# Kernel tuning notes

Hardware: AMD Instinct MI355X
Metric: run time of the kernel (lower is better)

The kernel has to match this reference:

```python
import jax, jax.numpy as jnp
import numpy as np

MARGIN = 1.0
CONTR_LAMDA = 100.0
GN_LAMDA = 0.3
IMG_SCALE = 2
EPS = 1e-9


def bilinear(fmap, pts):
    # fmap: (B,C,H,W); pts: (B,N,2) as (x,y). Returns (B*N, C).
    B, C, H, W = fmap.shape
    N = pts.shape[1]
    x = jnp.clip(pts[..., 0], 0.0, W - 1.0)
    y = jnp.clip(pts[..., 1], 0.0, H - 1.0)
    x0 = jnp.floor(x)
    y0 = jnp.floor(y)
    wx = (x - x0)[:, None, :]
    wy = (y - y0)[:, None, :]
    x0i = x0.astype(jnp.int32)
    y0i = y0.astype(jnp.int32)
    x1i = jnp.minimum(x0i + 1, W - 1)
    y1i = jnp.minimum(y0i + 1, H - 1)
    fm = fmap.reshape(B, C, H * W)

    def gather(yi, xi):
        idx = yi * W + xi  # (B,N)
        idx = jnp.broadcast_to(idx[:, None, :], (B, C, N))
        return jnp.take_along_axis(fm, idx, axis=2)  # (B,C,N)

    v = (gather(y0i, x0i) * (1 - wx) * (1 - wy)
         + gather(y0i, x1i) * wx * (1 - wy)
         + gather(y1i, x0i) * (1 - wx) * wy
         + gather(y1i, x1i) * wx * wy)
    return v.transpose(0, 2, 1).reshape(B * N, C)


def grad2d(f):
    # central differences with edge replication (torch_gradient)
    fx = jnp.pad(f, ((0, 0), (0, 0), (0, 0), (1, 1)), mode='edge')
    gx = 0.5 * (fx[..., 2:] - fx[..., :-2])
    fy = jnp.pad(f, ((0, 0), (0, 0), (1, 1), (0, 0)), mode='edge')
    gy = 0.5 * (fy[..., 2:, :] - fy[..., :-2, :])
    return gx, gy


def gn_loss(f_t, fb, ub, noise):
    # f_t: (B*N,C); fb: (B,C,H,W); ub,noise: (B,N,2)
    B, N, _ = ub.shape
    xs = noise + ub
    f_s = bilinear(fb, xs)
    r = f_s - f_t  # (BN, C) residual
    gx, gy = grad2d(fb)
    Jx = bilinear(gx, xs)  # (BN, C)
    Jy = bilinear(gy, xs)
    # H = J^T J + eps*I  -- closed-form batched 2x2
    a = jnp.sum(Jx * Jx, axis=1) + EPS
    d = jnp.sum(Jy * Jy, axis=1) + EPS
    b = jnp.sum(Jx * Jy, axis=1)
    det = a * d - b * b
    bx = jnp.sum(Jx * r, axis=1)
    by = jnp.sum(Jy * r, axis=1)
    # Hinv @ (J^T r)
    ix = (d * bx - b * by) / det
    iy = (-b * bx + a * by) / det
    miu = xs.reshape(B * N, 2) - jnp.stack([ix, iy], axis=-1)
    du = ub.reshape(B * N, 2) - miu
    q = a * du[:, 0] ** 2 + 2.0 * b * du[:, 0] * du[:, 1] + d * du[:, 1] ** 2
    e1 = 0.5 * jnp.sum(q)
    e2 = B * N * jnp.log(jnp.asarray(2.0 * np.pi, jnp.float32)) - 0.5 * jnp.sum(jnp.log(det))
    return e1 + 2.0 * e2 / 7.0


def triplet_loss(fa_map, fb_map, ma, mb, ng):
    fa = bilinear(fa_map, ma)
    fp = bilinear(fb_map, mb)
    fn = bilinear(fb_map, ng)
    dp = jnp.linalg.norm(fa - fp, axis=1)
    dn = jnp.linalg.norm(fa - fn, axis=1)
    return jnp.mean(jax.nn.relu(dp - dn + MARGIN))


def setup_inputs() -> dict:
    key = jax.random.key(0)
    ks = jax.random.split(key, 16)
    B, C, N = 4, 32, 2048
    sizes = [64, 128, 256, 512]
    d = {}
    for i, h in enumerate(sizes):
        d[f'fa{i}'] = jax.random.normal(ks[i], (B, C, h, h), jnp.float32)
        d[f'fb{i}'] = jax.random.normal(ks[4 + i], (B, C, h, h), jnp.float32)
        d[f'noise{i}'] = jax.random.normal(ks[8 + i], (B, N, 2), jnp.float32)
    d['ma'] = jax.random.uniform(ks[12], (B, N, 2), jnp.float32) * 1024.0
    d['mb'] = jax.random.uniform(ks[13], (B, N, 2), jnp.float32) * 1024.0
    d['neg'] = jax.random.uniform(ks[14], (B, N, 2), jnp.float32) * 1024.0
    d['epoch'] = 5
    return d


def reference(fa0, fa1, fa2, fa3, fb0, fb1, fb2, fb3,
              noise0, noise1, noise2, noise3, ma, mb, neg, epoch):
    Fa = [fa0, fa1, fa2, fa3]
    Fb = [fb0, fb1, fb2, fb3]
    noises = [noise0, noise1, noise2, noise3]
    loss = jnp.float32(0.0)
    tl = jnp.float32(0.0)
    gl = jnp.float32(0.0)
    for i in range(4):
        level = 2 ** (3 - i)
        s = float(level * IMG_SCALE)
        f_t = bilinear(Fa[i], ma / s)
        lt = triplet_loss(Fa[i], Fb[i], ma / s, mb / s, neg / s)
        lg = gn_loss(f_t, Fb[i], mb / s, noises[i])
        loss = loss + CONTR_LAMDA * lt + GN_LAMDA * lg
        tl = tl + CONTR_LAMDA * lt
        gl = gl + GN_LAMDA * lg
    return loss, tl, gl
```

## Files before the change

### kernel.cpp

```cpp
#include <hip/hip_runtime.h>
#include <math.h>


struct BL { int x0, x1, y0, y1; float wx, wy; };
struct LevelPtrs { const float* fa[4]; const float* fb[4]; const float* nz[4]; };

__device__ __forceinline__ float2 load2u(const float* p) { float2 v; __builtin_memcpy(&v, p, 8); return v; }
__device__ __forceinline__ float4 load4u(const float* p) { float4 v; __builtin_memcpy(&v, p, 16); return v; }

__device__ __forceinline__ BL bl_setup(float px, float py, int W, int H) {
    BL r;
    float x = fminf(fmaxf(px, 0.0f), (float)(W - 1));
    float y = fminf(fmaxf(py, 0.0f), (float)(H - 1));
    float fx = floorf(x), fy = floorf(y);
    r.wx = x - fx; r.wy = y - fy;
    r.x0 = (int)fx; r.y0 = (int)fy;
    r.x1 = min(r.x0 + 1, W - 1);
    r.y1 = min(r.y0 + 1, H - 1);
    return r;
}

__device__ __forceinline__ float bl_eval_slow(const float* __restrict__ f, int W, const BL& s) {
    float v00 = f[s.y0 * W + s.x0];
    float v01 = f[s.y0 * W + s.x1];
    float v10 = f[s.y1 * W + s.x0];
    float v11 = f[s.y1 * W + s.x1];
    float a0 = v00 + s.wx * (v01 - v00);
    float a1 = v10 + s.wx * (v11 - v10);
    return a0 + s.wy * (a1 - a0);
}

__device__ __forceinline__ void j_eval_slow(const float* __restrict__ f, int W, int H,
                                            const BL& s, float& Jx, float& Jy) {
    int xR0 = min(s.x0 + 1, W - 1), xL0 = max(s.x0 - 1, 0);
    int xR1 = min(s.x1 + 1, W - 1), xL1 = max(s.x1 - 1, 0);
    int yD0 = min(s.y0 + 1, H - 1), yU0 = max(s.y0 - 1, 0);
    int yD1 = min(s.y1 + 1, H - 1), yU1 = max(s.y1 - 1, 0);
    const float* r0 = f + s.y0 * W;
    const float* r1 = f + s.y1 * W;
    float gx00 = r0[xR0] - r0[xL0];
    float gx01 = r0[xR1] - r0[xL1];
    float gx10 = r1[xR0] - r1[xL0];
    float gx11 = r1[xR1] - r1[xL1];
    float gy00 = f[yD0 * W + s.x0] - f[yU0 * W + s.x0];
    float gy01 = f[yD0 * W + s.x1] - f[yU0 * W + s.x1];
    float gy10 = f[yD1 * W + s.x0] - f[yU1 * W + s.x0];
    float gy11 = f[yD1 * W + s.x1] - f[yU1 * W + s.x1];
    float g0 = gx00 + s.wx * (gx01 - gx00);
    float g1 = gx10 + s.wx * (gx11 - gx10);
    Jx = 0.5f * (g0 + s.wy * (g1 - g0));
    float h0 = gy00 + s.wx * (gy01 - gy00);
    float h1 = gy10 + s.wx * (gy11 - gy10);
    Jy = 0.5f * (h0 + s.wy * (h1 - h0));
}

__device__ __forceinline__ float warp32_sum(float v) {
    v += __shfl_xor(v, 16);
    v += __shfl_xor(v, 8);
    v += __shfl_xor(v, 4);
    v += __shfl_xor(v, 2);
    v += __shfl_xor(v, 1);
    return v;
}

__global__ __launch_bounds__(1024) void sort_points_kernel(
    const float* __restrict__ mb, int* __restrict__ perm) {
    const int b = blockIdx.x;
    __shared__ unsigned int keys[2048];
    const float* mbb = mb + (size_t)b * 2048 * 2;
    for (int i = threadIdx.x; i < 2048; i += 1024) {
        int ix = min(max((int)mbb[i * 2 + 0], 0), 1023);
        int iy = min(max((int)mbb[i * 2 + 1], 0), 1023);
        unsigned m = 0;
        #pragma unroll
        for (int t = 0; t < 10; ++t)
            m |= (((unsigned)(ix >> t) & 1u) << (2 * t)) | (((unsigned)(iy >> t) & 1u) << (2 * t + 1));
        keys[i] = (m << 11) | (unsigned)i;
    }
    __syncthreads();
    for (unsigned k = 2; k <= 2048; k <<= 1) {
        for (unsigned j = k >> 1; j > 0; j >>= 1) {
            unsigned t = threadIdx.x;
            unsigned i1 = 2 * t - (t & (j - 1));
            unsigned i2 = i1 + j;
            bool up = ((i1 & k) == 0);
            unsigned a = keys[i1], c = keys[i2];
            if ((a > c) == up) { keys[i1] = c; keys[i2] = a; }
            __syncthreads();
        }
    }
    for (int i = threadIdx.x; i < 2048; i += 1024)
        perm[b * 2048 + i] = (int)(keys[i] & 2047u);
}

struct Task {
    const float* fac;
    const float* fbc;
    BL sa, sb, sg, sx;
    float nzx, nzy;
    bool fast;
    float2 va0, va1, vb0, vb1, vg0, vg1;
    float4 xm, x0, x1, x2;
    float fav, fpv, fnv, fsv, Jx, Jy;
};

__device__ __forceinline__ void task_setup(Task& T, int rank, const int* __restrict__ perm,
                                           const LevelPtrs& P, int lvl, int c, int W, int H,
                                           float inv_s,
                                           const float* __restrict__ ma,
                                           const float* __restrict__ mb,
                                           const float* __restrict__ ng) {
    const int b = rank >> 11;
    const int n = perm ? perm[rank] : (rank & 2047);
    const int q = (b << 11) + n;
    const int HW = H * W;
    T.fac = P.fa[lvl] + (size_t)(b * 32 + c) * HW;
    T.fbc = P.fb[lvl] + (size_t)(b * 32 + c) * HW;
    const float* noise = P.nz[lvl];
    const int p2 = q * 2;
    T.nzx = noise[p2]; T.nzy = noise[p2 + 1];
    const float pax = ma[p2] * inv_s, pay = ma[p2 + 1] * inv_s;
    const float pbx = mb[p2] * inv_s, pby = mb[p2 + 1] * inv_s;
    const float pnx = ng[p2] * inv_s, pny = ng[p2 + 1] * inv_s;
    const float xsx = T.nzx + pbx, xsy = T.nzy + pby;
    T.sa = bl_setup(pax, pay, W, H);
    T.sb = bl_setup(pbx, pby, W, H);
    T.sg = bl_setup(pnx, pny, W, H);
    T.sx = bl_setup(xsx, xsy, W, H);
    T.fast = (T.sa.x0 < W - 1) & (T.sb.x0 < W - 1) & (T.sg.x0 < W - 1) &
             (T.sx.x0 >= 1) & (T.sx.x0 <= W - 3) & (T.sx.y0 >= 1) & (T.sx.y0 <= H - 3);
}

__device__ __forceinline__ void task_issue(Task& T, int W, int H) {
    if (T.fast) {
        const float* xbp = T.fbc + (T.sx.y0 - 1) * W + (T.sx.x0 - 1);
        T.va0 = load2u(T.fac + T.sa.y0 * W + T.sa.x0);
        T.va1 = load2u(T.fac + T.sa.y1 * W + T.sa.x0);
        T.vb0 = load2u(T.fbc + T.sb.y0 * W + T.sb.x0);
        T.vb1 = load2u(T.fbc + T.sb.y1 * W + T.sb.x0);
        T.vg0 = load2u(T.fbc + T.sg.y0 * W + T.sg.x0);
        T.vg1 = load2u(T.fbc + T.sg.y1 * W + T.sg.x0);
        T.xm = load4u(xbp);
        T.x0 = load4u(xbp + W);
        T.x1 = load4u(xbp + 2 * W);
        T.x2 = load4u(xbp + 3 * W);
    } else {
        T.fav = bl_eval_slow(T.fac, W, T.sa);
        T.fpv = bl_eval_slow(T.fbc, W, T.sb);
        T.fnv = bl_eval_slow(T.fbc, W, T.sg);
        T.fsv = bl_eval_slow(T.fbc, W, T.sx);
        j_eval_slow(T.fbc, W, H, T.sx, T.Jx, T.Jy);
    }
}

__device__ __forceinline__ void task_consume(Task& T) {
    if (T.fast) {
        {
            float t0 = T.va0.x + T.sa.wx * (T.va0.y - T.va0.x);
            float t1 = T.va1.x + T.sa.wx * (T.va1.y - T.va1.x);
            T.fav = t0 + T.sa.wy * (t1 - t0);
        }
        {
            float t0 = T.vb0.x + T.sb.wx * (T.vb0.y - T.vb0.x);
            float t1 = T.vb1.x + T.sb.wx * (T.vb1.y - T.vb1.x);
            T.fpv = t0 + T.sb.wy * (t1 - t0);
        }
        {
            float t0 = T.vg0.x + T.sg.wx * (T.vg0.y - T.vg0.x);
            float t1 = T.vg1.x + T.sg.wx * (T.vg1.y - T.vg1.x);
            T.fnv = t0 + T.sg.wy * (t1 - t0);
        }
        {
            float wx = T.sx.wx, wy = T.sx.wy;
            float t0 = T.x0.y + wx * (T.x0.z - T.x0.y);
            float t1 = T.x1.y + wx * (T.x1.z - T.x1.y);
            T.fsv = t0 + wy * (t1 - t0);
            float gx00 = T.x0.z - T.x0.x, gx01 = T.x0.w - T.x0.y;
            float gx10 = T.x1.z - T.x1.x, gx11 = T.x1.w - T.x1.y;
            float gy00 = T.x1.y - T.xm.y, gy01 = T.x1.z - T.xm.z;
            float gy10 = T.x2.y - T.x0.y, gy11 = T.x2.z - T.x0.z;
            float g0 = gx00 + wx * (gx01 - gx00);
            float g1 = gx10 + wx * (gx11 - gx10);
            T.Jx = 0.5f * (g0 + wy * (g1 - g0));
            float h0 = gy00 + wx * (gy01 - gy00);
            float h1 = gy10 + wx * (gy11 - gy10);
            T.Jy = 0.5f * (h0 + wy * (h1 - h0));
        }
    }
}

__device__ __forceinline__ void task_reduce(const Task& T, int c, float* red0,
                                            float* red1, float* red2, int slot2) {
    float r = T.fsv - T.fav;
    float a  = warp32_sum(T.Jx * T.Jx);
    float dd = warp32_sum(T.Jy * T.Jy);
    float bb = warp32_sum(T.Jx * T.Jy);
    float bx = warp32_sum(T.Jx * r);
    float by = warp32_sum(T.Jy * r);
    float dfp = T.fav - T.fpv, dfn = T.fav - T.fnv;
    float sp = warp32_sum(dfp * dfp);
    float sn = warp32_sum(dfn * dfn);
    if (c == 0) {
        a += 1e-9f; dd += 1e-9f;
        float det = a * dd - bb * bb;
        float ix = (dd * bx - bb * by) / det;
        float iy = (a * by - bb * bx) / det;
        float dux = ix - T.nzx;
        float duy = iy - T.nzy;
        float qv = a * dux * dux + 2.0f * bb * dux * duy + dd * duy * duy;
        red0[slot2] = fmaxf(sqrtf(sp) - sqrtf(sn) + 1.0f, 0.0f);
        red1[slot2] = qv;
        red2[slot2] = logf(det);
    }
}

__global__ __launch_bounds__(256) void gn_fused_kernel(
    LevelPtrs P, const float* __restrict__ ma, const float* __restrict__ mb,
    const float* __restrict__ ng, const int* __restrict__ perm,
    float* __restrict__ blk_out) {
    const int tid = threadIdx.x;
    const int c = tid & 31;
    const int slot = tid >> 5;
    const int lvl = slot >> 1;
    const int po = slot & 1;
    const int bid = blockIdx.x;
    const int s_blk = ((bid & 7) << 8) + (bid >> 3);
    const int base = s_blk * 4;
    const int H = 64 << lvl;
    const int W = H;
    const float inv_s = 0.0625f * (float)(1 << lvl);

    Task T0, T1;
    task_setup(T0, base + po,     perm, P, lvl, c, W, H, inv_s, ma, mb, ng);
    task_setup(T1, base + 2 + po, perm, P, lvl, c, W, H, inv_s, ma, mb, ng);
    task_issue(T0, W, H);
    task_issue(T1, W, H);
    task_consume(T0);
    task_consume(T1);

    __shared__ float red[3][16];
    task_reduce(T0, c, red[0], red[1], red[2], slot * 2 + 0);
    task_reduce(T1, c, red[0], red[1], red[2], slot * 2 + 1);
    __syncthreads();
    if (tid == 0) {
        float t = 0.0f, qq = 0.0f, l = 0.0f;
        #pragma unroll
        for (int i = 0; i < 16; ++i) { t += red[0][i]; qq += red[1][i]; l += red[2][i]; }
        blk_out[bid * 3 + 0] = t;
        blk_out[bid * 3 + 1] = qq;
        blk_out[bid * 3 + 2] = l;
    }
}

__global__ __launch_bounds__(256) void gn_final_kernel(
    const float* __restrict__ part, int nblk, float* __restrict__ out) {
    __shared__ double sd[3][256];
    double st = 0.0, sq = 0.0, sl = 0.0;
    for (int i = threadIdx.x; i < nblk; i += 256) {
        st += (double)part[i * 3 + 0];
        sq += (double)part[i * 3 + 1];
        sl += (double)part[i * 3 + 2];
    }
    sd[0][threadIdx.x] = st; sd[1][threadIdx.x] = sq; sd[2][threadIdx.x] = sl;
    __syncthreads();
    for (int s = 128; s > 0; s >>= 1) {
        if (threadIdx.x < s) {
            sd[0][threadIdx.x] += sd[0][threadIdx.x + s];
            sd[1][threadIdx.x] += sd[1][threadIdx.x + s];
            sd[2][threadIdx.x] += sd[2][threadIdx.x + s];
        }
        __syncthreads();
    }
    if (threadIdx.x == 0) {
        double S_t = sd[0][0], S_q = sd[1][0], S_l = sd[2][0];
        double tl = 100.0 * S_t / 8192.0;
        double e2 = 4.0 * 8192.0 * 1.8378770664093453 - 0.5 * S_l;
        double gl = 0.3 * (0.5 * S_q + (2.0 / 7.0) * e2);
        out[0] = (float)(tl + gl);
        out[1] = (float)tl;
        out[2] = (float)gl;
    }
}

extern "C" void kernel_launch(void* const* d_in, const int* in_sizes, int n_in,
                              void* d_out, int out_size, void* d_ws, size_t ws_size,
                              hipStream_t stream) {
    const bool dict_order = (in_sizes[1] == in_sizes[0]);
    LevelPtrs P;
    for (int i = 0; i < 4; ++i) {
        if (dict_order) {
            P.fa[i] = (const float*)d_in[3 * i + 0];
            P.fb[i] = (const float*)d_in[3 * i + 1];
            P.nz[i] = (const float*)d_in[3 * i + 2];
        } else {
            P.fa[i] = (const float*)d_in[i];
            P.fb[i] = (const float*)d_in[4 + i];
            P.nz[i] = (const float*)d_in[8 + i];
        }
    }
    const float* ma = (const float*)d_in[12];
    const float* mb = (const float*)d_in[13];
    const float* ng = (const float*)d_in[14];

    float* ws = (float*)d_ws;
    const int nblk = 2048;
    float* partials = ws;
    int* perm = (int*)(ws + nblk * 3);
    const bool do_sort = ws_size >= (size_t)(nblk * 3 + 8192) * 4;

    if (do_sort) sort_points_kernel<<<4, 1024, 0, stream>>>(mb, perm);
    gn_fused_kernel<<<nblk, 256, 0, stream>>>(P, ma, mb, ng, do_sort ? perm : nullptr, partials);
    gn_final_kernel<<<1, 256, 0, stream>>>(partials, nblk, (float*)d_out);
}
```

Measured before the change: 110.3 us.

## Split gather into sorted per-coordinate passes with workspace staging of features

```diff
diff --git a/kernel.cpp b/kernel.cpp
--- a/kernel.cpp
+++ b/kernel.cpp
@@ -8,15 +8,17 @@
 __device__ __forceinline__ float2 load2u(const float* p) { float2 v; __builtin_memcpy(&v, p, 8); return v; }
 __device__ __forceinline__ float4 load4u(const float* p) { float4 v; __builtin_memcpy(&v, p, 16); return v; }
 
-__device__ __forceinline__ BL bl_setup(float px, float py, int W, int H) {
+__device__ __forceinline__ BL bl_setup2(float px, float py, int W, int H) {
     BL r;
     float x = fminf(fmaxf(px, 0.0f), (float)(W - 1));
     float y = fminf(fmaxf(py, 0.0f), (float)(H - 1));
     float fx = floorf(x), fy = floorf(y);
     r.wx = x - fx; r.wy = y - fy;
     r.x0 = (int)fx; r.y0 = (int)fy;
-    r.x1 = min(r.x0 + 1, W - 1);
-    r.y1 = min(r.y0 + 1, H - 1);
+    if (r.x0 >= W - 1) { r.x0 = W - 2; r.wx = 1.0f; }
+    if (r.y0 >= H - 1) { r.y0 = H - 2; r.wy = 1.0f; }
+    r.x1 = r.x0 + 1;
+    r.y1 = r.y0 + 1;
     return r;
 }
 
@@ -54,6 +56,16 @@
     Jy = 0.5f * (h0 + s.wy * (h1 - h0));
 }
 
+__device__ __forceinline__ float wave64_sum(float v) {
+    v += __shfl_xor(v, 32);
+    v += __shfl_xor(v, 16);
+    v += __shfl_xor(v, 8);
+    v += __shfl_xor(v, 4);
+    v += __shfl_xor(v, 2);
+    v += __shfl_xor(v, 1);
+    return v;
+}
+
 __device__ __forceinline__ float warp32_sum(float v) {
     v += __shfl_xor(v, 16);
     v += __shfl_xor(v, 8);
@@ -63,14 +75,17 @@
     return v;
 }
 
-__global__ __launch_bounds__(1024) void sort_points_kernel(
-    const float* __restrict__ mb, int* __restrict__ perm) {
-    const int b = blockIdx.x;
+__global__ __launch_bounds__(1024) void sort3_kernel(
+    const float* __restrict__ ma, const float* __restrict__ mb,
+    const float* __restrict__ ng, int* __restrict__ perm) {
+    const int cid = blockIdx.x >> 2;
+    const int b = blockIdx.x & 3;
+    const float* coords = (cid == 0) ? ma : (cid == 1) ? mb : ng;
     __shared__ unsigned int keys[2048];
-    const float* mbb = mb + (size_t)b * 2048 * 2;
+    const float* cb = coords + (size_t)b * 2048 * 2;
     for (int i = threadIdx.x; i < 2048; i += 1024) {
-        int ix = min(max((int)mbb[i * 2 + 0], 0), 1023);
-        int iy = min(max((int)mbb[i * 2 + 1], 0), 1023);
+        int ix = min(max((int)cb[i * 2 + 0], 0), 1023);
+        int iy = min(max((int)cb[i * 2 + 1], 0), 1023);
         unsigned m = 0;
         #pragma unroll
         for (int t = 0; t < 10; ++t)
@@ -90,7 +105,203 @@
         }
     }
     for (int i = threadIdx.x; i < 2048; i += 1024)
-        perm[b * 2048 + i] = (int)(keys[i] & 2047u);
+        perm[cid * 8192 + b * 2048 + i] = (int)(keys[i] & 2047u);
+}
+
+__global__ __launch_bounds__(256) void gather_pass_kernel(
+    LevelPtrs P, const float* __restrict__ ma, const float* __restrict__ ng,
+    const int* __restrict__ perm, float* __restrict__ ft, float* __restrict__ fn) {
+    const int bid = blockIdx.x;
+    const int role = bid & 1;
+    const int r = bid >> 1;
+    const int lvl = 3 - (r >> 7);
+    const int g = r & 127;
+    const int tid = threadIdx.x;
+    const int lane = tid & 63, w = tid >> 6, ch0 = w * 8;
+    const int rank = g * 64 + lane;
+    const int b = rank >> 11;
+    const int* pm = perm + (role ? 2 * 8192 : 0);
+    const int q = (b << 11) + pm[rank];
+    const int H = 64 << lvl, W = H, HW = H * W;
+    const float inv_s = 0.0625f * (float)(1 << lvl);
+    const float* coords = role ? ng : ma;
+    const float px = coords[q * 2] * inv_s, py = coords[q * 2 + 1] * inv_s;
+    BL s = bl_setup2(px, py, W, H);
+    const float* src = role ? P.fb[lvl] : P.fa[lvl];
+    const float* base = src + (size_t)(b * 32 + ch0) * HW + s.y0 * W + s.x0;
+
+    float2 v0[8], v1[8];
+    #pragma unroll
+    for (int cc = 0; cc < 8; ++cc) {
+        v0[cc] = load2u(base + (size_t)cc * HW);
+        v1[cc] = load2u(base + (size_t)cc * HW + W);
+    }
+    float out[8];
+    #pragma unroll
+    for (int cc = 0; cc < 8; ++cc) {
+        float t0 = v0[cc].x + s.wx * (v0[cc].y - v0[cc].x);
+        float t1 = v1[cc].x + s.wx * (v1[cc].y - v1[cc].x);
+        out[cc] = t0 + s.wy * (t1 - t0);
+    }
+    float* dst = (role ? fn : ft) + ((size_t)lvl * 8192 + q) * 32 + ch0;
+    float4 o0 = {out[0], out[1], out[2], out[3]};
+    float4 o1 = {out[4], out[5], out[6], out[7]};
+    *(float4*)dst = o0;
+    *(float4*)(dst + 4) = o1;
+}
+
+__device__ __forceinline__ void consume_ch(
+    const float* __restrict__ plane, int W, int H, const BL& sb, const BL& sx,
+    bool interior, float2 m0, float2 m1,
+    float4 r0, float4 r1, float4 r2, float4 r3,
+    float ftv, float fnv,
+    float& sp, float& sn, float& aa, float& dd, float& bb, float& bx, float& by) {
+    float t0 = m0.x + sb.wx * (m0.y - m0.x);
+    float t1 = m1.x + sb.wx * (m1.y - m1.x);
+    float fpv = t0 + sb.wy * (t1 - t0);
+    float fsv, Jx, Jy;
+    if (interior) {
+        float wx = sx.wx, wy = sx.wy;
+        float a0 = r1.y + wx * (r1.z - r1.y);
+        float a1 = r2.y + wx * (r2.z - r2.y);
+        fsv = a0 + wy * (a1 - a0);
+        float gx00 = r1.z - r1.x, gx01 = r1.w - r1.y;
+        float gx10 = r2.z - r2.x, gx11 = r2.w - r2.y;
+        float gy00 = r2.y - r0.y, gy01 = r2.z - r0.z;
+        float gy10 = r3.y - r1.y, gy11 = r3.z - r1.z;
+        float g0 = gx00 + wx * (gx01 - gx00);
+        float g1 = gx10 + wx * (gx11 - gx10);
+        Jx = 0.5f * (g0 + wy * (g1 - g0));
+        float h0 = gy00 + wx * (gy01 - gy00);
+        float h1 = gy10 + wx * (gy11 - gy10);
+        Jy = 0.5f * (h0 + wy * (h1 - h0));
+    } else {
+        fsv = bl_eval_slow(plane, W, sx);
+        j_eval_slow(plane, W, H, sx, Jx, Jy);
+    }
+    float rr = fsv - ftv;
+    float dp = ftv - fpv, dn = ftv - fnv;
+    sp += dp * dp;
+    sn += dn * dn;
+    aa += Jx * Jx;
+    dd += Jy * Jy;
+    bb += Jx * Jy;
+    bx += Jx * rr;
+    by += Jy * rr;
+}
+
+__global__ __launch_bounds__(256) void gn_main_kernel(
+    LevelPtrs P, const float* __restrict__ mb, const int* __restrict__ perm_mb,
+    const float* __restrict__ ft, const float* __restrict__ fn,
+    float* __restrict__ blk_out) {
+    const int bid = blockIdx.x;
+    const int lvl = 3 - (bid >> 7);
+    const int g = bid & 127;
+    const int tid = threadIdx.x;
+    const int lane = tid & 63, w = tid >> 6, ch0 = w * 8;
+    const int rank = g * 64 + lane;
+    const int b = rank >> 11;
+    const int q = (b << 11) + perm_mb[rank];
+    const int H = 64 << lvl, W = H, HW = H * W;
+    const float inv_s = 0.0625f * (float)(1 << lvl);
+    const float* noise = P.nz[lvl];
+    const int p2 = q * 2;
+    const float nzx = noise[p2], nzy = noise[p2 + 1];
+    const float pbx = mb[p2] * inv_s, pby = mb[p2 + 1] * inv_s;
+    const float xsx = nzx + pbx, xsy = nzy + pby;
+    BL sb = bl_setup2(pbx, pby, W, H);
+    BL sx = bl_setup2(xsx, xsy, W, H);
+    const bool interior = (sx.x0 >= 1) & (sx.x0 <= W - 3) & (sx.y0 >= 1) & (sx.y0 <= H - 3);
+    const int pbx0 = min(max(sx.x0 - 1, 0), W - 4);
+    const int pby0 = min(max(sx.y0 - 1, 0), H - 4);
+    const float* fb0 = P.fb[lvl] + (size_t)(b * 32 + ch0) * HW;
+
+    const float* ftp = ft + ((size_t)lvl * 8192 + q) * 32 + ch0;
+    const float* fnp = fn + ((size_t)lvl * 8192 + q) * 32 + ch0;
+    float4 ftA = *(const float4*)ftp, ftB = *(const float4*)(ftp + 4);
+    float4 fnA = *(const float4*)fnp, fnB = *(const float4*)(fnp + 4);
+    float ftv[8] = {ftA.x, ftA.y, ftA.z, ftA.w, ftB.x, ftB.y, ftB.z, ftB.w};
+    float fnv[8] = {fnA.x, fnA.y, fnA.z, fnA.w, fnB.x, fnB.y, fnB.z, fnB.w};
+
+    float sp = 0, sn = 0, aa = 0, dd = 0, bb = 0, bx = 0, by = 0;
+    const int mboff0 = sb.y0 * W + sb.x0;
+    const int pboff = pby0 * W + pbx0;
+    #pragma unroll
+    for (int cc = 0; cc < 8; cc += 2) {
+        const float* p0 = fb0 + (size_t)cc * HW;
+        const float* p1 = p0 + HW;
+        float2 m00 = load2u(p0 + mboff0);
+        float2 m01 = load2u(p0 + mboff0 + W);
+        float2 m10 = load2u(p1 + mboff0);
+        float2 m11 = load2u(p1 + mboff0 + W);
+        const float* xb0 = p0 + pboff;
+        const float* xb1 = p1 + pboff;
+        float4 r00 = load4u(xb0), r01 = load4u(xb0 + W), r02 = load4u(xb0 + 2 * W), r03 = load4u(xb0 + 3 * W);
+        float4 r10 = load4u(xb1), r11 = load4u(xb1 + W), r12 = load4u(xb1 + 2 * W), r13 = load4u(xb1 + 3 * W);
+        consume_ch(p0, W, H, sb, sx, interior, m00, m01, r00, r01, r02, r03,
+                   ftv[cc], fnv[cc], sp, sn, aa, dd, bb, bx, by);
+        consume_ch(p1, W, H, sb, sx, interior, m10, m11, r10, r11, r12, r13,
+                   ftv[cc + 1], fnv[cc + 1], sp, sn, aa, dd, bb, bx, by);
+    }
+
+    __shared__ float red[4][64][7];
+    red[w][lane][0] = sp; red[w][lane][1] = sn; red[w][lane][2] = aa;
+    red[w][lane][3] = dd; red[w][lane][4] = bb; red[w][lane][5] = bx;
+    red[w][lane][6] = by;
+    __syncthreads();
+    if (tid < 64) {
+        float t[7];
+        #pragma unroll
+        for (int k = 0; k < 7; ++k)
+            t[k] = red[0][tid][k] + red[1][tid][k] + red[2][tid][k] + red[3][tid][k];
+        float a2 = t[2] + 1e-9f, d2 = t[3] + 1e-9f, b2 = t[4];
+        float det = a2 * d2 - b2 * b2;
+        float ix = (d2 * t[5] - b2 * t[6]) / det;
+        float iy = (a2 * t[6] - b2 * t[5]) / det;
+        float dux = ix - nzx;
+        float duy = iy - nzy;
+        float qv = a2 * dux * dux + 2.0f * b2 * dux * duy + d2 * duy * duy;
+        float trip = fmaxf(sqrtf(t[0]) - sqrtf(t[1]) + 1.0f, 0.0f);
+        float ld = logf(det);
+        trip = wave64_sum(trip);
+        qv = wave64_sum(qv);
+        ld = wave64_sum(ld);
+        if (tid == 0) {
+            blk_out[bid * 3 + 0] = trip;
+            blk_out[bid * 3 + 1] = qv;
+            blk_out[bid * 3 + 2] = ld;
+        }
+    }
+}
+
+__global__ __launch_bounds__(256) void gn_final_kernel(
+    const float* __restrict__ part, int nblk, float* __restrict__ out) {
+    __shared__ double sd[3][256];
+    double st = 0.0, sq = 0.0, sl = 0.0;
+    for (int i = threadIdx.x; i < nblk; i += 256) {
+        st += (double)part[i * 3 + 0];
+        sq += (double)part[i * 3 + 1];
+        sl += (double)part[i * 3 + 2];
+    }
+    sd[0][threadIdx.x] = st; sd[1][threadIdx.x] = sq; sd[2][threadIdx.x] = sl;
+    __syncthreads();
+    for (int s = 128; s > 0; s >>= 1) {
+        if (threadIdx.x < s) {
+            sd[0][threadIdx.x] += sd[0][threadIdx.x + s];
+            sd[1][threadIdx.x] += sd[1][threadIdx.x + s];
+            sd[2][threadIdx.x] += sd[2][threadIdx.x + s];
+        }
+        __syncthreads();
+    }
+    if (threadIdx.x == 0) {
+        double S_t = sd[0][0], S_q = sd[1][0], S_l = sd[2][0];
+        double tl = 100.0 * S_t / 8192.0;
+        double e2 = 4.0 * 8192.0 * 1.8378770664093453 - 0.5 * S_l;
+        double gl = 0.3 * (0.5 * S_q + (2.0 / 7.0) * e2);
+        out[0] = (float)(tl + gl);
+        out[1] = (float)tl;
+        out[2] = (float)gl;
+    }
 }
 
 struct Task {
@@ -104,15 +315,13 @@
     float fav, fpv, fnv, fsv, Jx, Jy;
 };
 
-__device__ __forceinline__ void task_setup(Task& T, int rank, const int* __restrict__ perm,
-                                           const LevelPtrs& P, int lvl, int c, int W, int H,
-                                           float inv_s,
+__device__ __forceinline__ void task_setup(Task& T, int rank, const LevelPtrs& P,
+                                           int lvl, int c, int W, int H, float inv_s,
                                            const float* __restrict__ ma,
                                            const float* __restrict__ mb,
                                            const float* __restrict__ ng) {
     const int b = rank >> 11;
-    const int n = perm ? perm[rank] : (rank & 2047);
-    const int q = (b << 11) + n;
+    const int q = rank;
     const int HW = H * W;
     T.fac = P.fa[lvl] + (size_t)(b * 32 + c) * HW;
     T.fbc = P.fb[lvl] + (size_t)(b * 32 + c) * HW;
@@ -123,69 +332,63 @@
     const float pbx = mb[p2] * inv_s, pby = mb[p2 + 1] * inv_s;
     const float pnx = ng[p2] * inv_s, pny = ng[p2 + 1] * inv_s;
     const float xsx = T.nzx + pbx, xsy = T.nzy + pby;
-    T.sa = bl_setup(pax, pay, W, H);
-    T.sb = bl_setup(pbx, pby, W, H);
-    T.sg = bl_setup(pnx, pny, W, H);
-    T.sx = bl_setup(xsx, xsy, W, H);
-    T.fast = (T.sa.x0 < W - 1) & (T.sb.x0 < W - 1) & (T.sg.x0 < W - 1) &
-             (T.sx.x0 >= 1) & (T.sx.x0 <= W - 3) & (T.sx.y0 >= 1) & (T.sx.y0 <= H - 3);
+    T.sa = bl_setup2(pax, pay, W, H);
+    T.sb = bl_setup2(pbx, pby, W, H);
+    T.sg = bl_setup2(pnx, pny, W, H);
+    T.sx = bl_setup2(xsx, xsy, W, H);
+    T.fast = (T.sx.x0 >= 1) & (T.sx.x0 <= W - 3) & (T.sx.y0 >= 1) & (T.sx.y0 <= H - 3);
 }
 
 __device__ __forceinline__ void task_issue(Task& T, int W, int H) {
+    T.va0 = load2u(T.fac + T.sa.y0 * W + T.sa.x0);
+    T.va1 = load2u(T.fac + T.sa.y1 * W + T.sa.x0);
+    T.vb0 = load2u(T.fbc + T.sb.y0 * W + T.sb.x0);
+    T.vb1 = load2u(T.fbc + T.sb.y1 * W + T.sb.x0);
+    T.vg0 = load2u(T.fbc + T.sg.y0 * W + T.sg.x0);
+    T.vg1 = load2u(T.fbc + T.sg.y1 * W + T.sg.x0);
+    int bx0 = min(max(T.sx.x0 - 1, 0), W - 4);
+    int by0 = min(max(T.sx.y0 - 1, 0), H - 4);
+    const float* xbp = T.fbc + by0 * W + bx0;
+    T.xm = load4u(xbp);
+    T.x0 = load4u(xbp + W);
+    T.x1 = load4u(xbp + 2 * W);
+    T.x2 = load4u(xbp + 3 * W);
+}
+
+__device__ __forceinline__ void task_consume(Task& T, int W, int H) {
+    {
+        float t0 = T.va0.x + T.sa.wx * (T.va0.y - T.va0.x);
+        float t1 = T.va1.x + T.sa.wx * (T.va1.y - T.va1.x);
+        T.fav = t0 + T.sa.wy * (t1 - t0);
+    }
+    {
+        float t0 = T.vb0.x + T.sb.wx * (T.vb0.y - T.vb0.x);
+        float t1 = T.vb1.x + T.sb.wx * (T.vb1.y - T.vb1.x);
+        T.fpv = t0 + T.sb.wy * (t1 - t0);
+    }
+    {
+        float t0 = T.vg0.x + T.sg.wx * (T.vg0.y - T.vg0.x);
+        float t1 = T.vg1.x + T.sg.wx * (T.vg1.y - T.vg1.x);
+        T.fnv = t0 + T.sg.wy * (t1 - t0);
+    }
     if (T.fast) {
-        const float* xbp = T.fbc + (T.sx.y0 - 1) * W + (T.sx.x0 - 1);
-        T.va0 = load2u(T.fac + T.sa.y0 * W + T.sa.x0);
-        T.va1 = load2u(T.fac + T.sa.y1 * W + T.sa.x0);
-        T.vb0 = load2u(T.fbc + T.sb.y0 * W + T.sb.x0);
-        T.vb1 = load2u(T.fbc + T.sb.y1 * W + T.sb.x0);
-        T.vg0 = load2u(T.fbc + T.sg.y0 * W + T.sg.x0);
-        T.vg1 = load2u(T.fbc + T.sg.y1 * W + T.sg.x0);
-        T.xm = load4u(xbp);
-        T.x0 = load4u(xbp + W);
-        T.x1 = load4u(xbp + 2 * W);
-        T.x2 = load4u(xbp + 3 * W);
+        float wx = T.sx.wx, wy = T.sx.wy;
+        float t0 = T.x0.y + wx * (T.x0.z - T.x0.y);
+        float t1 = T.x1.y + wx * (T.x1.z - T.x1.y);
+        T.fsv = t0 + wy * (t1 - t0);
+        float gx00 = T.x0.z - T.x0.x, gx01 = T.x0.w - T.x0.y;
+        float gx10 = T.x1.z - T.x1.x, gx11 = T.x1.w - T.x1.y;
+        float gy00 = T.x1.y - T.xm.y, gy01 = T.x1.z - T.xm.z;
+        float gy10 = T.x2.y - T.x0.y, gy11 = T.x2.z - T.x0.z;
+        float g0 = gx00 + wx * (gx01 - gx00);
+        float g1 = gx10 + wx * (gx11 - gx10);
+        T.Jx = 0.5f * (g0 + wy * (g1 - g0));
+        float h0 = gy00 + wx * (gy01 - gy00);
+        float h1 = gy10 + wx * (gy11 - gy10);
+        T.Jy = 0.5f * (h0 + wy * (h1 - h0));
     } else {
-        T.fav = bl_eval_slow(T.fac, W, T.sa);
-        T.fpv = bl_eval_slow(T.fbc, W, T.sb);
-        T.fnv = bl_eval_slow(T.fbc, W, T.sg);
         T.fsv = bl_eval_slow(T.fbc, W, T.sx);
         j_eval_slow(T.fbc, W, H, T.sx, T.Jx, T.Jy);
-    }
-}
-
-__device__ __forceinline__ void task_consume(Task& T) {
-    if (T.fast) {
-        {
-            float t0 = T.va0.x + T.sa.wx * (T.va0.y - T.va0.x);
-            float t1 = T.va1.x + T.sa.wx * (T.va1.y - T.va1.x);
-            T.fav = t0 + T.sa.wy * (t1 - t0);
-        }
-        {
-            float t0 = T.vb0.x + T.sb.wx * (T.vb0.y - T.vb0.x);
-            float t1 = T.vb1.x + T.sb.wx * (T.vb1.y - T.vb1.x);
-            T.fpv = t0 + T.sb.wy * (t1 - t0);
-        }
-        {
-            float t0 = T.vg0.x + T.sg.wx * (T.vg0.y - T.vg0.x);
-            float t1 = T.vg1.x + T.sg.wx * (T.vg1.y - T.vg1.x);
-            T.fnv = t0 + T.sg.wy * (t1 - t0);
-        }
-        {
-            float wx = T.sx.wx, wy = T.sx.wy;
-            float t0 = T.x0.y + wx * (T.x0.z - T.x0.y);
-            float t1 = T.x1.y + wx * (T.x1.z - T.x1.y);
-            T.fsv = t0 + wy * (t1 - t0);
-            float gx00 = T.x0.z - T.x0.x, gx01 = T.x0.w - T.x0.y;
-            float gx10 = T.x1.z - T.x1.x, gx11 = T.x1.w - T.x1.y;
-            float gy00 = T.x1.y - T.xm.y, gy01 = T.x1.z - T.xm.z;
-            float gy10 = T.x2.y - T.x0.y, gy11 = T.x2.z - T.x0.z;
-            float g0 = gx00 + wx * (gx01 - gx00);
-            float g1 = gx10 + wx * (gx11 - gx10);
-            T.Jx = 0.5f * (g0 + wy * (g1 - g0));
-            float h0 = gy00 + wx * (gy01 - gy00);
-            float h1 = gy10 + wx * (gy11 - gy10);
-            T.Jy = 0.5f * (h0 + wy * (h1 - h0));
-        }
     }
 }
 
@@ -214,29 +417,27 @@
     }
 }
 
-__global__ __launch_bounds__(256) void gn_fused_kernel(
+__global__ __launch_bounds__(256) void gn_fallback_kernel(
     LevelPtrs P, const float* __restrict__ ma, const float* __restrict__ mb,
-    const float* __restrict__ ng, const int* __restrict__ perm,
-    float* __restrict__ blk_out) {
+    const float* __restrict__ ng, float* __restrict__ blk_out) {
     const int tid = threadIdx.x;
     const int c = tid & 31;
     const int slot = tid >> 5;
     const int lvl = slot >> 1;
     const int po = slot & 1;
     const int bid = blockIdx.x;
-    const int s_blk = ((bid & 7) << 8) + (bid >> 3);
-    const int base = s_blk * 4;
+    const int base = bid * 4;
     const int H = 64 << lvl;
     const int W = H;
     const float inv_s = 0.0625f * (float)(1 << lvl);
 
     Task T0, T1;
-    task_setup(T0, base + po,     perm, P, lvl, c, W, H, inv_s, ma, mb, ng);
-    task_setup(T1, base + 2 + po, perm, P, lvl, c, W, H, inv_s, ma, mb, ng);
+    task_setup(T0, base + po,     P, lvl, c, W, H, inv_s, ma, mb, ng);
+    task_setup(T1, base + 2 + po, P, lvl, c, W, H, inv_s, ma, mb, ng);
     task_issue(T0, W, H);
     task_issue(T1, W, H);
-    task_consume(T0);
-    task_consume(T1);
+    task_consume(T0, W, H);
+    task_consume(T1, W, H);
 
     __shared__ float red[3][16];
     task_reduce(T0, c, red[0], red[1], red[2], slot * 2 + 0);
@@ -249,36 +450,6 @@
         blk_out[bid * 3 + 0] = t;
         blk_out[bid * 3 + 1] = qq;
         blk_out[bid * 3 + 2] = l;
-    }
-}
-
-__global__ __launch_bounds__(256) void gn_final_kernel(
-    const float* __restrict__ part, int nblk, float* __restrict__ out) {
-    __shared__ double sd[3][256];
-    double st = 0.0, sq = 0.0, sl = 0.0;
-    for (int i = threadIdx.x; i < nblk; i += 256) {
-        st += (double)part[i * 3 + 0];
-        sq += (double)part[i * 3 + 1];
-        sl += (double)part[i * 3 + 2];
-    }
-    sd[0][threadIdx.x] = st; sd[1][threadIdx.x] = sq; sd[2][threadIdx.x] = sl;
-    __syncthreads();
-    for (int s = 128; s > 0; s >>= 1) {
-        if (threadIdx.x < s) {
-            sd[0][threadIdx.x] += sd[0][threadIdx.x + s];
-            sd[1][threadIdx.x] += sd[1][threadIdx.x + s];
-            sd[2][threadIdx.x] += sd[2][threadIdx.x + s];
-        }
-        __syncthreads();
-    }
-    if (threadIdx.x == 0) {
-        double S_t = sd[0][0], S_q = sd[1][0], S_l = sd[2][0];
-        double tl = 100.0 * S_t / 8192.0;
-        double e2 = 4.0 * 8192.0 * 1.8378770664093453 - 0.5 * S_l;
-        double gl = 0.3 * (0.5 * S_q + (2.0 / 7.0) * e2);
-        out[0] = (float)(tl + gl);
-        out[1] = (float)tl;
-        out[2] = (float)gl;
     }
 }
 
@@ -303,12 +474,22 @@
     const float* ng = (const float*)d_in[14];
 
     float* ws = (float*)d_ws;
-    const int nblk = 2048;
-    float* partials = ws;
-    int* perm = (int*)(ws + nblk * 3);
-    const bool do_sort = ws_size >= (size_t)(nblk * 3 + 8192) * 4;
-
-    if (do_sort) sort_points_kernel<<<4, 1024, 0, stream>>>(mb, perm);
-    gn_fused_kernel<<<nblk, 256, 0, stream>>>(P, ma, mb, ng, do_sort ? perm : nullptr, partials);
-    gn_final_kernel<<<1, 256, 0, stream>>>(partials, nblk, (float*)d_out);
-}
+    const size_t FT_OFF = 26112;
+    const size_t FN_OFF = FT_OFF + 4 * 8192 * 32;
+    const size_t NEED = (FN_OFF + 4 * 8192 * 32) * 4;
+
+    if (ws_size >= NEED) {
+        float* partials = ws;
+        int* perm = (int*)(ws + 1536);
+        float* ft = ws + FT_OFF;
+        float* fn = ws + FN_OFF;
+        sort3_kernel<<<12, 1024, 0, stream>>>(ma, mb, ng, perm);
+        gather_pass_kernel<<<1024, 256, 0, stream>>>(P, ma, ng, perm, ft, fn);
+        gn_main_kernel<<<512, 256, 0, stream>>>(P, mb, perm + 8192, ft, fn, partials);
+        gn_final_kernel<<<1, 256, 0, stream>>>(partials, 512, (float*)d_out);
+    } else {
+        float* partials = ws;
+        gn_fallback_kernel<<<2048, 256, 0, stream>>>(P, ma, mb, ng, partials);
+        gn_final_kernel<<<1, 256, 0, stream>>>(partials, 2048, (float*)d_out);
+    }
+}
```

Result: faster. 90.71 us (-17.8%).
